# Kernel optimization log

Measured on AMD Instinct MI355X. Metric: run time of the kernel, lower is better.

The kernel has to match this reference:

```python
import jax, jax.numpy as jnp
import numpy as np

NUM_INPUTS, NUM_HIDDEN, NUM_OUTPUTS = 512, 1024, 35
T, B = 100, 512
N_HID_LAYERS = 4  # number of hidden Leaky layers (num_layers)
SLOPE = 25.0      # snntorch surrogate.fast_sigmoid default slope
BETA, THR = 0.95, 1.0


@jax.custom_vjp
def spike(x):
    # Heaviside forward, fast-sigmoid surrogate backward
    return (x > 0).astype(x.dtype)

def _spike_fwd(x):
    return (x > 0).astype(x.dtype), x

def _spike_bwd(x, g):
    return (g / (SLOPE * jnp.abs(x) + 1.0) ** 2,)

spike.defvjp(_spike_fwd, _spike_bwd)


def leaky(x, mem, beta, thr):
    # snntorch Leaky, reset_mechanism='subtract':
    # reset computed from PREVIOUS mem (detached), then decay+input, then fire
    reset = jax.lax.stop_gradient((mem - thr > 0).astype(x.dtype))
    mem = jnp.clip(beta, 0.0, 1.0) * mem + x - reset * thr
    spk = spike(mem - thr)
    return spk, mem


def setup_inputs() -> dict:
    key = jax.random.key(0)
    ks = jax.random.split(key, 8)
    data = jax.random.normal(ks[0], (T, B, NUM_INPUTS), dtype=jnp.float32)
    s_in = 1.0 / np.sqrt(NUM_INPUTS)
    s_h = 1.0 / np.sqrt(NUM_HIDDEN)
    W_in = jax.random.uniform(ks[1], (NUM_HIDDEN, NUM_INPUTS), minval=-s_in, maxval=s_in, dtype=jnp.float32)
    b_in = jax.random.uniform(ks[2], (NUM_HIDDEN,), minval=-s_in, maxval=s_in, dtype=jnp.float32)
    W_h = jax.random.uniform(ks[3], (N_HID_LAYERS - 1, NUM_HIDDEN, NUM_HIDDEN), minval=-s_h, maxval=s_h, dtype=jnp.float32)
    b_h = jax.random.uniform(ks[4], (N_HID_LAYERS - 1, NUM_HIDDEN), minval=-s_h, maxval=s_h, dtype=jnp.float32)
    W_out = jax.random.uniform(ks[5], (NUM_OUTPUTS, NUM_HIDDEN), minval=-s_h, maxval=s_h, dtype=jnp.float32)
    b_out = jax.random.uniform(ks[6], (NUM_OUTPUTS,), minval=-s_h, maxval=s_h, dtype=jnp.float32)
    # learn_beta/learn_threshold: each Leaky holds its own (identically initialized) params
    beta_h = jnp.full((N_HID_LAYERS, NUM_HIDDEN), BETA, dtype=jnp.float32)
    thr_h = jnp.full((N_HID_LAYERS, NUM_HIDDEN), THR, dtype=jnp.float32)
    beta_o = jnp.full((NUM_OUTPUTS,), BETA, dtype=jnp.float32)
    thr_o = jnp.full((NUM_OUTPUTS,), THR, dtype=jnp.float32)
    return {"data": data, "W_in": W_in, "b_in": b_in, "W_h": W_h, "b_h": b_h,
            "W_out": W_out, "b_out": b_out, "beta_h": beta_h, "thr_h": thr_h,
            "beta_o": beta_o, "thr_o": thr_o, "timestep": 100}


def reference(data, W_in, b_in, W_h, b_h, W_out, b_out, beta_h, thr_h, beta_o, thr_o, timestep):
    n_hid = beta_h.shape[0]
    Bsz = data.shape[1]

    def step(mems, x_t):
        new_mems = []
        x = x_t @ W_in.T + b_in
        x, m = leaky(x, mems[0], beta_h[0], thr_h[0])
        new_mems.append(m)
        for i in range(n_hid - 1):
            z = x @ W_h[i].T + b_h[i]
            x, m = leaky(z, mems[i + 1], beta_h[i + 1], thr_h[i + 1])
            new_mems.append(m)
        z = x @ W_out.T + b_out
        spk, m = leaky(z, mems[n_hid], beta_o, thr_o)
        new_mems.append(m)
        return tuple(new_mems), spk

    mems0 = tuple([jnp.zeros((Bsz, NUM_HIDDEN), dtype=data.dtype) for _ in range(n_hid)]
                  + [jnp.zeros((Bsz, NUM_OUTPUTS), dtype=data.dtype)])
    _, spk_rec = jax.lax.scan(step, mems0, data[:timestep])
    return spk_rec  # [T, B, num_outputs]
```

## Files before the change

kernel.cpp:

```cpp
#include <hip/hip_runtime.h>
#include <hip/hip_bf16.h>


#define NB 512
#define NH 1024
#define NI 512
#define NO 35
#define TT 100
#define NT 8
#define BITFRAME 16384

typedef __bf16 bf16x8 __attribute__((ext_vector_type(8)));
typedef float f32x4 __attribute__((ext_vector_type(4)));
typedef int   i32x4 __attribute__((ext_vector_type(4)));

__device__ __forceinline__ size_t tiled_off(int row, int k, int KT) {
    return ((size_t)((row >> 4) * KT + (k >> 5)) * 64
            + (row & 15) + (((k >> 3) & 3) << 4)) * 8 + (k & 7);
}

__device__ __forceinline__ void leaky_upd(float zin, float mprev, float be, float th,
                                          float& mnew, float& spk) {
    float rs = (mprev - th > 0.0f) ? th : 0.0f;
    float bc = fminf(fmaxf(be, 0.0f), 1.0f);
    mnew = bc * mprev + zin - rs;
    spk  = (mnew - th > 0.0f) ? 1.0f : 0.0f;
}

#define WS_MEM123   0u
#define WS_MEM0     6291456u
#define WS_MEMO     8388608u
#define WS_FLAGS    8486912u
#define WS_GEN      8487936u
#define WS_RING0    8488192u
#define WS_RING1    9536768u
#define WS_RING2    10585344u
#define WS_RING3    11633920u
#define WS_W8       12682496u
#define WS_WIT      25265408u
#define WS_WOT      28411136u
#define WS_Z0       28706048u
#define STEP_BYTES  2097152u

__global__ __launch_bounds__(256)
void split_weights_i8(const float* __restrict__ W_h, signed char* __restrict__ W8) {
    const int id = blockIdx.x * 256 + threadIdx.x;
    const int layer = id >> 16;
    const int rem = id & 65535;
    const int n = rem >> 6;
    const int k0 = (rem & 63) << 4;
    const float* src = W_h + ((size_t)layer * NH + n) * NH + k0;
    const int kq = k0 >> 4;
    const int ck = kq >> 2;
    const int lane = (n & 15) | ((kq & 3) << 4);
    signed char* dstL = W8 + (size_t)layer * 4 * NH * NH;
    const size_t gb = ((size_t)(n >> 4) * 16 + ck) * 1024 + lane * 16;

    signed char q1[16], q2[16], q3[16], q4[16];
    #pragma unroll
    for (int j = 0; j < 16; ++j) {
        float w = src[j];
        float f1 = rintf(w * 0x1p11f);   float r1 = w  - f1 * 0x1p-11f;
        float f2 = rintf(r1 * 0x1p18f);  float r2 = r1 - f2 * 0x1p-18f;
        float f3 = rintf(r2 * 0x1p25f);  float r3 = r2 - f3 * 0x1p-25f;
        float f4 = rintf(r3 * 0x1p32f);
        q1[j] = (signed char)(int)f1; q2[j] = (signed char)(int)f2;
        q3[j] = (signed char)(int)f3; q4[j] = (signed char)(int)f4;
    }
    #pragma unroll
    for (int j = 0; j < 16; ++j) {
        dstL[(size_t)0 * 64 * 16384 + gb + j] = q1[j];
        dstL[(size_t)1 * 64 * 16384 + gb + j] = q2[j];
        dstL[(size_t)2 * 64 * 16384 + gb + j] = q3[j];
        dstL[(size_t)3 * 64 * 16384 + gb + j] = q4[j];
    }
}

__global__ __launch_bounds__(256)
void split_win(const float* __restrict__ W_in, __bf16* __restrict__ Wi_t) {
    const int id = blockIdx.x * 256 + threadIdx.x;
    const int n = id >> 6;
    const int k0 = (id & 63) << 3;
    const float* src = W_in + (size_t)n * NI + k0;
    const size_t PS = (size_t)NH * NI;
    const size_t off = tiled_off(n, k0, 16);
    bf16x8 p1, p2, p3;
    #pragma unroll
    for (int j = 0; j < 8; ++j) {
        float w = src[j];
        __bf16 a = (__bf16)w;  float r1 = w - (float)a;
        __bf16 b = (__bf16)r1; float r2 = r1 - (float)b;
        __bf16 c = (__bf16)r2;
        p1[j] = a; p2[j] = b; p3[j] = c;
    }
    *reinterpret_cast<bf16x8*>(Wi_t + 0 * PS + off) = p1;
    *reinterpret_cast<bf16x8*>(Wi_t + 1 * PS + off) = p2;
    *reinterpret_cast<bf16x8*>(Wi_t + 2 * PS + off) = p3;
}

__global__ __launch_bounds__(256)
void split_wout(const float* __restrict__ W_out, __bf16* __restrict__ Wo_t) {
    const int id = blockIdx.x * 256 + threadIdx.x;
    if (id >= 48 * 128) return;
    const int o = id >> 7;
    const int k0 = (id & 127) << 3;
    const size_t PS = (size_t)48 * NH;
    const size_t off = tiled_off(o, k0, 32);
    bf16x8 p1 = {}, p2 = {}, p3 = {};
    if (o < NO) {
        const float* src = W_out + (size_t)o * NH + k0;
        #pragma unroll
        for (int j = 0; j < 8; ++j) {
            float w = src[j];
            __bf16 a = (__bf16)w;  float r1 = w - (float)a;
            __bf16 b = (__bf16)r1; float r2 = r1 - (float)b;
            __bf16 c = (__bf16)r2;
            p1[j] = a; p2[j] = b; p3[j] = c;
        }
    }
    *reinterpret_cast<bf16x8*>(Wo_t + 0 * PS + off) = p1;
    *reinterpret_cast<bf16x8*>(Wo_t + 1 * PS + off) = p2;
    *reinterpret_cast<bf16x8*>(Wo_t + 2 * PS + off) = p3;
}

__global__ __launch_bounds__(256)
void z0_gemm(const float* __restrict__ X,
             const __bf16* __restrict__ Wi_t,
             const float* __restrict__ bias,
             float* __restrict__ Z0)
{
    const int tid = threadIdx.x;
    const int lane = tid & 63;
    const int w = tid >> 6;
    const int wm = w >> 1, wn = w & 1;
    const int m_base = blockIdx.y * 64 + wm * 32;
    const int n_base = blockIdx.x * 64 + wn * 32;
    const size_t PS = (size_t)NH * NI;

    f32x4 acc[2][2] = {};
    const float* asrc[2];
    #pragma unroll
    for (int mt = 0; mt < 2; ++mt)
        asrc[mt] = X + (size_t)(m_base + mt * 16 + (lane & 15)) * NI + ((lane >> 4) << 3);

    float4 c0[2], c1[2];
    #pragma unroll
    for (int mt = 0; mt < 2; ++mt) {
        c0[mt] = *reinterpret_cast<const float4*>(asrc[mt]);
        c1[mt] = *reinterpret_cast<const float4*>(asrc[mt] + 4);
    }

    for (int kt = 0; kt < 16; ++kt) {
        float4 n0[2], n1[2];
        if (kt < 15) {
            #pragma unroll
            for (int mt = 0; mt < 2; ++mt) {
                n0[mt] = *reinterpret_cast<const float4*>(asrc[mt] + (kt + 1) * 32);
                n1[mt] = *reinterpret_cast<const float4*>(asrc[mt] + (kt + 1) * 32 + 4);
            }
        }
        bf16x8 a1[2], a2[2], a3[2];
        #pragma unroll
        for (int mt = 0; mt < 2; ++mt) {
            float xv[8] = {c0[mt].x, c0[mt].y, c0[mt].z, c0[mt].w,
                           c1[mt].x, c1[mt].y, c1[mt].z, c1[mt].w};
            #pragma unroll
            for (int j = 0; j < 8; ++j) {
                float x = xv[j];
                __bf16 h1 = (__bf16)x;  float r1 = x - (float)h1;
                __bf16 h2 = (__bf16)r1; float r2 = r1 - (float)h2;
                __bf16 h3 = (__bf16)r2;
                a1[mt][j] = h1; a2[mt][j] = h2; a3[mt][j] = h3;
            }
        }
        #pragma unroll
        for (int nt = 0; nt < 2; ++nt) {
            const size_t bo = ((size_t)(((n_base >> 4) + nt) * 16 + kt) * 64 + lane) * 8;
            bf16x8 b1 = *reinterpret_cast<const bf16x8*>(Wi_t + bo);
            bf16x8 b2 = *reinterpret_cast<const bf16x8*>(Wi_t + PS + bo);
            bf16x8 b3 = *reinterpret_cast<const bf16x8*>(Wi_t + 2 * PS + bo);
            #pragma unroll
            for (int mt = 0; mt < 2; ++mt) {
                f32x4 A = acc[mt][nt];
                A = __builtin_amdgcn_mfma_f32_16x16x32_bf16(a1[mt], b1, A, 0, 0, 0);
                A = __builtin_amdgcn_mfma_f32_16x16x32_bf16(a1[mt], b2, A, 0, 0, 0);
                A = __builtin_amdgcn_mfma_f32_16x16x32_bf16(a2[mt], b1, A, 0, 0, 0);
                A = __builtin_amdgcn_mfma_f32_16x16x32_bf16(a2[mt], b2, A, 0, 0, 0);
                A = __builtin_amdgcn_mfma_f32_16x16x32_bf16(a1[mt], b3, A, 0, 0, 0);
                A = __builtin_amdgcn_mfma_f32_16x16x32_bf16(a3[mt], b1, A, 0, 0, 0);
                acc[mt][nt] = A;
            }
        }
        if (kt < 15) {
            #pragma unroll
            for (int mt = 0; mt < 2; ++mt) { c0[mt] = n0[mt]; c1[mt] = n1[mt]; }
        }
    }

    const int c = lane & 15;
    const int r0 = (lane >> 4) * 4;
    #pragma unroll
    for (int nt = 0; nt < 2; ++nt) {
        const int n = n_base + nt * 16 + c;
        const float bi = bias[n];
        #pragma unroll
        for (int mt = 0; mt < 2; ++mt) {
            #pragma unroll
            for (int r = 0; r < 4; ++r) {
                const int m = m_base + mt * 16 + r0 + r;
                const int tl = m >> 9, b = m & 511;
                Z0[(size_t)tl * (NB * NH) + tiled_off(b, n, 32)] = acc[mt][nt][r] + bi;
            }
        }
    }
}

__device__ __forceinline__ void gridbar(int* flags, int* gen, int target) {
    __syncthreads();
    if (threadIdx.x == 0) {
        __builtin_amdgcn_fence(__ATOMIC_RELEASE, "agent");
        __hip_atomic_store(&flags[blockIdx.x], target, __ATOMIC_RELAXED, __HIP_MEMORY_SCOPE_AGENT);
    }
    if (blockIdx.x == 0) {
        if (threadIdx.x < 64) {
            const int l = threadIdx.x;
            for (;;) {
                int v0 = __hip_atomic_load(&flags[l],       __ATOMIC_RELAXED, __HIP_MEMORY_SCOPE_AGENT);
                int v1 = __hip_atomic_load(&flags[l + 64],  __ATOMIC_RELAXED, __HIP_MEMORY_SCOPE_AGENT);
                int v2 = __hip_atomic_load(&flags[l + 128], __ATOMIC_RELAXED, __HIP_MEMORY_SCOPE_AGENT);
                int v3 = __hip_atomic_load(&flags[l + 192], __ATOMIC_RELAXED, __HIP_MEMORY_SCOPE_AGENT);
                int mn = min(min(v0, v1), min(v2, v3));
                if (__all(mn >= target)) break;
                __builtin_amdgcn_s_sleep(1);
            }
        }
        __syncthreads();
        if (threadIdx.x == 0) {
            __builtin_amdgcn_fence(__ATOMIC_ACQ_REL, "agent");
            __hip_atomic_store(gen, target, __ATOMIC_RELAXED, __HIP_MEMORY_SCOPE_AGENT);
        }
    } else if (threadIdx.x == 0) {
        while (__hip_atomic_load(gen, __ATOMIC_RELAXED, __HIP_MEMORY_SCOPE_AGENT) < target)
            __builtin_amdgcn_s_sleep(2);
    }
    __syncthreads();
    __builtin_amdgcn_fence(__ATOMIC_ACQUIRE, "agent");
}

template<int NS>
__device__ __forceinline__ void hidden_run_i8(
    const unsigned int* const* Xp, unsigned short* const* Yp,
    const signed char* Wl, int cs, int rh, int w, int lane,
    float (&memr)[2][2][4], const float (&bi)[2], const float (&be)[2],
    const float (&th)[2])
{
    const int row  = lane & 15;
    const int lg   = lane >> 4;
    const int wsel = lg >> 1;
    const int hsel = (lg & 1) * 16;

    i32x4 acc[NS][2][2][4] = {};

    unsigned int bw[NS][2];
    #pragma unroll
    for (int q = 0; q < NS; ++q)
        #pragma unroll
        for (int i = 0; i < 2; ++i)
            bw[q][i] = Xp[q][((rh * 16 + w * 2 + i) * 32 + wsel) * 16 + row];

    for (int ck = 0; ck < 16; ++ck) {
        unsigned int nb[NS][2];
        if (ck < 15) {
            #pragma unroll
            for (int q = 0; q < NS; ++q)
                #pragma unroll
                for (int i = 0; i < 2; ++i)
                    nb[q][i] = Xp[q][((rh * 16 + w * 2 + i) * 32 + (ck + 1) * 2 + wsel) * 16 + row];
        }
        i32x4 bf[8];
        #pragma unroll
        for (int pn = 0; pn < 8; ++pn)
            bf[pn] = *reinterpret_cast<const i32x4*>(Wl + pn * 16384 + ck * 1024 + lane * 16);

        #pragma unroll
        for (int q = 0; q < NS; ++q) {
            #pragma unroll
            for (int i = 0; i < 2; ++i) {
                unsigned int half = (bw[q][i] >> hsel) & 0xFFFFu;
                union { unsigned int u[4]; i32x4 v; } a;
                a.u[0] = (((half      ) & 0xFu) * 0x204081u) & 0x01010101u;
                a.u[1] = (((half >>  4) & 0xFu) * 0x204081u) & 0x01010101u;
                a.u[2] = (((half >>  8) & 0xFu) * 0x204081u) & 0x01010101u;
                a.u[3] = (((half >> 12) & 0xFu) * 0x204081u) & 0x01010101u;
                #pragma unroll
                for (int nt = 0; nt < 2; ++nt)
                    #pragma unroll
                    for (int p = 0; p < 4; ++p)
                        acc[q][i][nt][p] = __builtin_amdgcn_mfma_i32_16x16x64_i8(
                            a.v, bf[p * 2 + nt], acc[q][i][nt][p], 0, 0, 0);
            }
        }
        if (ck < 15) {
            #pragma unroll
            for (int q = 0; q < NS; ++q) { bw[q][0] = nb[q][0]; bw[q][1] = nb[q][1]; }
        }
    }

    #pragma unroll
    for (int q = 0; q < NS; ++q) {
        #pragma unroll
        for (int i = 0; i < 2; ++i) {
            #pragma unroll
            for (int nt = 0; nt < 2; ++nt) {
                #pragma unroll
                for (int r = 0; r < 4; ++r) {
                    float z = (float)acc[q][i][nt][3][r] * 0x1p-32f
                            + (float)acc[q][i][nt][2][r] * 0x1p-25f;
                    z += (float)acc[q][i][nt][1][r] * 0x1p-18f;
                    z += (float)acc[q][i][nt][0][r] * 0x1p-11f;
                    float mn, sp;
                    leaky_upd(z + bi[nt], memr[i][nt][r], be[nt], th[nt], mn, sp);
                    memr[i][nt][r] = mn;
                    unsigned long long bal = __ballot(sp != 0.0f);
                    if ((lane & 15) == 0) {
                        const int rr = (lane >> 4) * 4 + r;
                        Yp[q][(((rh * 16 + w * 2 + i) * 32 + cs) * 16 + rr) * 2 + nt] =
                            (unsigned short)((bal >> ((lane >> 4) * 16)) & 0xFFFFu);
                    }
                }
            }
        }
    }
}

__global__ __launch_bounds__(512, 1)
void snn_pipe(const float* __restrict__ Z0,
              const signed char* __restrict__ W8,
              const __bf16* __restrict__ Wo_t,
              const float* __restrict__ b_h,
              const float* __restrict__ b_out,
              const float* __restrict__ beta_h,
              const float* __restrict__ thr_h,
              const float* __restrict__ beta_o,
              const float* __restrict__ thr_o,
              float* __restrict__ mem123,
              float* __restrict__ mem0_g,
              float* __restrict__ memo_g,
              unsigned int* __restrict__ ring0, unsigned int* __restrict__ ring1,
              unsigned int* __restrict__ ring2, unsigned int* __restrict__ ring3,
              float* __restrict__ out,
              int* __restrict__ flags, int* __restrict__ gen,
              int t0, int tc)
{
    __shared__ signed char Wl[8 * 16 * 1024];
    __shared__ unsigned long long lut[16];

    const int blk  = blockIdx.x;
    const int tid  = threadIdx.x;
    const int lane = tid & 63;
    const int w    = tid >> 6;

    if (tid < 16) {
        unsigned int lo = ((tid & 1) ? 0x3F80u : 0u) | ((tid & 2) ? 0x3F800000u : 0u);
        unsigned int hi = ((tid & 4) ? 0x3F80u : 0u) | ((tid & 8) ? 0x3F800000u : 0u);
        lut[tid] = ((unsigned long long)hi << 32) | lo;
    }

    const int G = (tc + NT - 1) / NT;

    if (blk < 192) {
        const int ell = blk >> 6;
        const int cs  = (blk & 63) >> 1;
        const int rh  = blk & 1;
        {
            const signed char* Wsrc = W8 + (size_t)ell * 4 * NH * NH;
            for (int idx = tid; idx < 8 * 1024; idx += 512) {
                const int pn = idx >> 10, off = idx & 1023;
                const int p = pn >> 1, nt = pn & 1;
                *reinterpret_cast<int4*>(Wl + pn * 16384 + off * 16) =
                    *reinterpret_cast<const int4*>(
                        Wsrc + (size_t)(p * 64 + cs * 2 + nt) * 16384 + off * 16);
            }
        }

        const int c = lane & 15;
        const int r0v = (lane >> 4) * 4;
        float* memg = mem123 + (size_t)ell * (NB * NH);
        float bi[2], be[2], th[2];
        #pragma unroll
        for (int nt = 0; nt < 2; ++nt) {
            const int n = cs * 32 + nt * 16 + c;
            bi[nt] = b_h[ell * NH + n];
            be[nt] = beta_h[(ell + 1) * NH + n];
            th[nt] = thr_h[(ell + 1) * NH + n];
        }
        float memr[2][2][4];
        #pragma unroll
        for (int i = 0; i < 2; ++i)
            #pragma unroll
            for (int nt = 0; nt < 2; ++nt)
                #pragma unroll
                for (int r = 0; r < 4; ++r)
                    memr[i][nt][r] = memg[(size_t)(rh * 256 + (w * 2 + i) * 16 + r0v + r) * NH
                                          + cs * 32 + nt * 16 + c];

        const unsigned int* rin = (ell == 0) ? ring0 : (ell == 1) ? ring1 : ring2;
        unsigned int* rout      = (ell == 0) ? ring1 : (ell == 1) ? ring2 : ring3;

        __syncthreads();

        for (int p = 0; p < G + 4; ++p) {
            const int g = p - 1 - ell;
            if (g >= 0 && g < G) {
                const int sbase = g * NT;
                const int send  = (sbase + NT < tc) ? sbase + NT : tc;
                const int slot0 = (g & 1) * NT;
                int s = sbase;
                while (s < send) {
                    const int base = slot0 + (s - sbase);
                    const unsigned int* Xp[2];
                    unsigned short* Yp[2];
                    if (send - s >= 2) {
                        #pragma unroll
                        for (int q = 0; q < 2; ++q) {
                            Xp[q] = rin + (size_t)(base + q) * BITFRAME;
                            Yp[q] = (unsigned short*)(rout + (size_t)(base + q) * BITFRAME);
                        }
                        hidden_run_i8<2>(Xp, Yp, Wl, cs, rh, w, lane, memr, bi, be, th);
                        s += 2;
                    } else {
                        Xp[0] = rin + (size_t)base * BITFRAME;
                        Yp[0] = (unsigned short*)(rout + (size_t)base * BITFRAME);
                        hidden_run_i8<1>(Xp, Yp, Wl, cs, rh, w, lane, memr, bi, be, th);
                        s += 1;
                    }
                }
            }
            gridbar(flags, gen, p + 1);
        }

        #pragma unroll
        for (int i = 0; i < 2; ++i)
            #pragma unroll
            for (int nt = 0; nt < 2; ++nt)
                #pragma unroll
                for (int r = 0; r < 4; ++r)
                    memg[(size_t)(rh * 256 + (w * 2 + i) * 16 + r0v + r) * NH
                         + cs * 32 + nt * 16 + c] = memr[i][nt][r];
    } else if (blk < 224) {
        const bool outw = (w < 3);
        const int omt = blk - 192;
        const int ont = w;
        const int c = lane & 15, r0v = (lane >> 4) * 4;
        const int row = lane & 15, sh2 = (lane >> 4) * 8;
        const int oo = ont * 16 + c;
        const size_t OPS = (size_t)48 * NH;
        float mo[4] = {0.f, 0.f, 0.f, 0.f};
        float obi = 0.f, obe = 0.f, oth = 1.f;
        if (outw && oo < NO) {
            obi = b_out[oo]; obe = beta_o[oo]; oth = thr_o[oo];
            #pragma unroll
            for (int r = 0; r < 4; ++r) mo[r] = memo_g[(omt * 16 + r0v + r) * NO + oo];
        }
        __syncthreads();

        for (int p = 0; p < G + 4; ++p) {
            if (outw) {
                const int go = p - 4;
                if (go >= 0 && go < G) {
                    const int sbase = go * NT;
                    const int send  = (sbase + NT < tc) ? sbase + NT : tc;
                    const int slot0 = (go & 1) * NT;
                    for (int s = sbase; s < send; ++s) {
                        const unsigned int* Xw =
                            ring3 + (size_t)(slot0 + s - sbase) * BITFRAME;
                        f32x4 acc = {};
                        for (int kt = 0; kt < 32; ++kt) {
                            unsigned int by = (Xw[(omt * 32 + kt) * 16 + row] >> sh2) & 0xffu;
                            union { unsigned long long u[2]; bf16x8 v; } a;
                            a.u[0] = lut[by & 15u];
                            a.u[1] = lut[by >> 4];
                            const size_t bo = ((size_t)(ont * 32 + kt) * 64 + lane) * 8;
                            bf16x8 q1 = *reinterpret_cast<const bf16x8*>(Wo_t + bo);
                            bf16x8 q2 = *reinterpret_cast<const bf16x8*>(Wo_t + OPS + bo);
                            bf16x8 q3 = *reinterpret_cast<const bf16x8*>(Wo_t + 2 * OPS + bo);
                            acc = __builtin_amdgcn_mfma_f32_16x16x32_bf16(a.v, q1, acc, 0, 0, 0);
                            acc = __builtin_amdgcn_mfma_f32_16x16x32_bf16(a.v, q2, acc, 0, 0, 0);
                            acc = __builtin_amdgcn_mfma_f32_16x16x32_bf16(a.v, q3, acc, 0, 0, 0);
                        }
                        if (oo < NO) {
                            #pragma unroll
                            for (int r = 0; r < 4; ++r) {
                                float mn, sp;
                                leaky_upd(acc[r] + obi, mo[r], obe, oth, mn, sp);
                                mo[r] = mn;
                                out[((size_t)(t0 + s) * NB + omt * 16 + r0v + r) * NO + oo] = sp;
                            }
                        }
                    }
                }
            }
            gridbar(flags, gen, p + 1);
        }

        if (outw && oo < NO) {
            #pragma unroll
            for (int r = 0; r < 4; ++r) memo_g[(omt * 16 + r0v + r) * NO + oo] = mo[r];
        }
    } else {
        const int wi   = (blk - 224) * 512 + tid;
        const int mtb  = wi >> 9;
        const int ktb  = (wi >> 4) & 31;
        const int i0   = (mtb * 32 + ktb) * 512 + (wi & 15) * 8;

        float m0[32], be0[32], th0[32];
        #pragma unroll
        for (int byt = 0; byt < 4; ++byt)
            #pragma unroll
            for (int j = 0; j < 8; ++j) {
                m0[byt * 8 + j]  = mem0_g[i0 + byt * 128 + j];
                be0[byt * 8 + j] = beta_h[ktb * 32 + byt * 8 + j];
                th0[byt * 8 + j] = thr_h[ktb * 32 + byt * 8 + j];
            }
        __syncthreads();

        for (int p = 0; p < G + 4; ++p) {
            if (p < G) {
                const int sbase = p * NT;
                const int send  = (sbase + NT < tc) ? sbase + NT : tc;
                const int slot0 = (p & 1) * NT;
                for (int s = sbase; s < send; ++s) {
                    const float* zs = Z0 + (size_t)s * (NB * NH) + i0;
                    float4 zv[8];
                    #pragma unroll
                    for (int byt = 0; byt < 4; ++byt) {
                        zv[byt * 2]     = *reinterpret_cast<const float4*>(zs + byt * 128);
                        zv[byt * 2 + 1] = *reinterpret_cast<const float4*>(zs + byt * 128 + 4);
                    }
                    unsigned int bits = 0;
                    #pragma unroll
                    for (int e = 0; e < 32; ++e) {
                        float z = reinterpret_cast<const float*>(zv)[e];
                        float mn, sp;
                        leaky_upd(z, m0[e], be0[e], th0[e], mn, sp);
                        m0[e] = mn;
                        bits |= (sp != 0.0f ? 1u : 0u) << e;
                    }
                    ring0[(size_t)(slot0 + s - sbase) * BITFRAME + wi] = bits;
                }
            }
            gridbar(flags, gen, p + 1);
        }

        #pragma unroll
        for (int byt = 0; byt < 4; ++byt)
            #pragma unroll
            for (int j = 0; j < 8; ++j)
                mem0_g[i0 + byt * 128 + j] = m0[byt * 8 + j];
    }
}

extern "C" void kernel_launch(void* const* d_in, const int* in_sizes, int n_in,
                              void* d_out, int out_size, void* d_ws, size_t ws_size,
                              hipStream_t stream) {
    const float* data   = (const float*)d_in[0];
    const float* W_in   = (const float*)d_in[1];
    const float* b_in   = (const float*)d_in[2];
    const float* W_h    = (const float*)d_in[3];
    const float* b_h    = (const float*)d_in[4];
    const float* W_out  = (const float*)d_in[5];
    const float* b_out  = (const float*)d_in[6];
    const float* beta_h = (const float*)d_in[7];
    const float* thr_h  = (const float*)d_in[8];
    const float* beta_o = (const float*)d_in[9];
    const float* thr_o  = (const float*)d_in[10];
    float* out = (float*)d_out;

    char* ws = (char*)d_ws;
    float*        mem123 = (float*)(ws + WS_MEM123);
    float*        mem0_g = (float*)(ws + WS_MEM0);
    float*        memo_g = (float*)(ws + WS_MEMO);
    int*          flags  = (int*)(ws + WS_FLAGS);
    int*          gen    = (int*)(ws + WS_GEN);
    unsigned int* ring0  = (unsigned int*)(ws + WS_RING0);
    unsigned int* ring1  = (unsigned int*)(ws + WS_RING1);
    unsigned int* ring2  = (unsigned int*)(ws + WS_RING2);
    unsigned int* ring3  = (unsigned int*)(ws + WS_RING3);
    signed char*  W8     = (signed char*)(ws + WS_W8);
    __bf16*       Wi_t   = (__bf16*)(ws + WS_WIT);
    __bf16*       Wo_t   = (__bf16*)(ws + WS_WOT);
    float*        Z0     = (float*)(ws + WS_Z0);

    size_t avail = (ws_size > WS_Z0) ? (ws_size - WS_Z0) / STEP_BYTES : 1;
    int Tc = (int)(avail < 1 ? 1 : (avail > TT ? TT : avail));

    hipMemsetAsync(ws, 0, WS_FLAGS, stream);
    split_weights_i8<<<dim3(768), dim3(256), 0, stream>>>(W_h, W8);
    split_win<<<dim3(256), dim3(256), 0, stream>>>(W_in, Wi_t);
    split_wout<<<dim3(24), dim3(256), 0, stream>>>(W_out, Wo_t);

    for (int t0c = 0; t0c < TT; t0c += Tc) {
        const int tcc = (TT - t0c < Tc) ? (TT - t0c) : Tc;
        z0_gemm<<<dim3(NH / 64, tcc * (NB / 64)), dim3(256), 0, stream>>>(
            data + (size_t)t0c * NB * NI, Wi_t, b_in, Z0);
        hipMemsetAsync(ws + WS_FLAGS, 0, 1280, stream);
        snn_pipe<<<dim3(256), dim3(512), 0, stream>>>(
            Z0, W8, Wo_t, b_h, b_out, beta_h, thr_h, beta_o, thr_o,
            mem123, mem0_g, memo_g, ring0, ring1, ring2, ring3, out,
            flags, gen, t0c, tcc);
    }
}
```

Baseline: 1.679 ms.

## Switch hidden-layer int8 MFMA to 32x32x32 tiles and pair output timesteps

The hidden-layer int8 GEMM moves from 16x16x64 MFMA tiles to 32x32x32 tiles. This changes the weight pre-split layout, the LDS weight staging, the accumulator and membrane register layout, and the spike bit-packing, which now writes 32-bit words instead of 16-bit halves. Each wave now covers 32 rows by 32 columns per tile, which is meant to halve the B-operand LDS reads per MFMA and cut the activation unpacking done per matrix op. The output-layer loop also processes two timesteps per pass so each loaded W_out fragment is reused. The risk is higher accumulator register pressure (16-wide i32 accumulators for each of NS and 4 splits) and possible LDS bank conflicts in the new layout.

```diff
diff --git a/kernel.cpp b/kernel.cpp
--- a/kernel.cpp
+++ b/kernel.cpp
@@ -13,6 +13,7 @@
 typedef __bf16 bf16x8 __attribute__((ext_vector_type(8)));
 typedef float f32x4 __attribute__((ext_vector_type(4)));
 typedef int   i32x4 __attribute__((ext_vector_type(4)));
+typedef int   i32x16 __attribute__((ext_vector_type(16)));
 
 __device__ __forceinline__ size_t tiled_off(int row, int k, int KT) {
     return ((size_t)((row >> 4) * KT + (k >> 5)) * 64
@@ -48,13 +49,13 @@
     const int layer = id >> 16;
     const int rem = id & 65535;
     const int n = rem >> 6;
-    const int k0 = (rem & 63) << 4;
+    const int kq = rem & 63;
+    const int k0 = kq << 4;
     const float* src = W_h + ((size_t)layer * NH + n) * NH + k0;
-    const int kq = k0 >> 4;
-    const int ck = kq >> 2;
-    const int lane = (n & 15) | ((kq & 3) << 4);
+    const int ck = kq >> 1;
+    const int lane = (n & 31) | ((kq & 1) << 5);
+    const int g = n >> 5;
     signed char* dstL = W8 + (size_t)layer * 4 * NH * NH;
-    const size_t gb = ((size_t)(n >> 4) * 16 + ck) * 1024 + lane * 16;
 
     signed char q1[16], q2[16], q3[16], q4[16];
     #pragma unroll
@@ -69,10 +70,10 @@
     }
     #pragma unroll
     for (int j = 0; j < 16; ++j) {
-        dstL[(size_t)0 * 64 * 16384 + gb + j] = q1[j];
-        dstL[(size_t)1 * 64 * 16384 + gb + j] = q2[j];
-        dstL[(size_t)2 * 64 * 16384 + gb + j] = q3[j];
-        dstL[(size_t)3 * 64 * 16384 + gb + j] = q4[j];
+        dstL[((size_t)(0 * 32 + g) * 32 + ck) * 1024 + lane * 16 + j] = q1[j];
+        dstL[((size_t)(1 * 32 + g) * 32 + ck) * 1024 + lane * 16 + j] = q2[j];
+        dstL[((size_t)(2 * 32 + g) * 32 + ck) * 1024 + lane * 16 + j] = q3[j];
+        dstL[((size_t)(3 * 32 + g) * 32 + ck) * 1024 + lane * 16 + j] = q4[j];
     }
 }
 
@@ -249,85 +250,70 @@
 
 template<int NS>
 __device__ __forceinline__ void hidden_run_i8(
-    const unsigned int* const* Xp, unsigned short* const* Yp,
+    const unsigned int* const* Xp, unsigned int* const* Yp,
     const signed char* Wl, int cs, int rh, int w, int lane,
-    float (&memr)[2][2][4], const float (&bi)[2], const float (&be)[2],
-    const float (&th)[2])
+    float (&memr)[16], float bi, float be, float th)
 {
-    const int row  = lane & 15;
-    const int lg   = lane >> 4;
-    const int wsel = lg >> 1;
-    const int hsel = (lg & 1) * 16;
-
-    i32x4 acc[NS][2][2][4] = {};
-
-    unsigned int bw[NS][2];
+    const int r32  = lane & 31;
+    const int khal = lane >> 5;
+    const int gr   = rh * 256 + w * 32 + r32;
+    const int mt   = gr >> 4;
+    const int r16  = gr & 15;
+    const int hsh  = khal * 16;
+
+    i32x16 acc[NS][4] = {};
+    unsigned int bw[NS];
     #pragma unroll
     for (int q = 0; q < NS; ++q)
-        #pragma unroll
-        for (int i = 0; i < 2; ++i)
-            bw[q][i] = Xp[q][((rh * 16 + w * 2 + i) * 32 + wsel) * 16 + row];
-
-    for (int ck = 0; ck < 16; ++ck) {
-        unsigned int nb[NS][2];
-        if (ck < 15) {
+        bw[q] = Xp[q][(mt * 32) * 16 + r16];
+
+    for (int ck = 0; ck < 32; ++ck) {
+        unsigned int nb[NS];
+        if (ck < 31) {
             #pragma unroll
             for (int q = 0; q < NS; ++q)
-                #pragma unroll
-                for (int i = 0; i < 2; ++i)
-                    nb[q][i] = Xp[q][((rh * 16 + w * 2 + i) * 32 + (ck + 1) * 2 + wsel) * 16 + row];
-        }
-        i32x4 bf[8];
-        #pragma unroll
-        for (int pn = 0; pn < 8; ++pn)
-            bf[pn] = *reinterpret_cast<const i32x4*>(Wl + pn * 16384 + ck * 1024 + lane * 16);
+                nb[q] = Xp[q][(mt * 32 + ck + 1) * 16 + r16];
+        }
+        i32x4 bf[4];
+        #pragma unroll
+        for (int p = 0; p < 4; ++p)
+            bf[p] = *reinterpret_cast<const i32x4*>(Wl + (size_t)(p * 32 + ck) * 1024 + lane * 16);
 
         #pragma unroll
         for (int q = 0; q < NS; ++q) {
-            #pragma unroll
-            for (int i = 0; i < 2; ++i) {
-                unsigned int half = (bw[q][i] >> hsel) & 0xFFFFu;
-                union { unsigned int u[4]; i32x4 v; } a;
-                a.u[0] = (((half      ) & 0xFu) * 0x204081u) & 0x01010101u;
-                a.u[1] = (((half >>  4) & 0xFu) * 0x204081u) & 0x01010101u;
-                a.u[2] = (((half >>  8) & 0xFu) * 0x204081u) & 0x01010101u;
-                a.u[3] = (((half >> 12) & 0xFu) * 0x204081u) & 0x01010101u;
-                #pragma unroll
-                for (int nt = 0; nt < 2; ++nt)
-                    #pragma unroll
-                    for (int p = 0; p < 4; ++p)
-                        acc[q][i][nt][p] = __builtin_amdgcn_mfma_i32_16x16x64_i8(
-                            a.v, bf[p * 2 + nt], acc[q][i][nt][p], 0, 0, 0);
-            }
-        }
-        if (ck < 15) {
-            #pragma unroll
-            for (int q = 0; q < NS; ++q) { bw[q][0] = nb[q][0]; bw[q][1] = nb[q][1]; }
+            unsigned int half = (bw[q] >> hsh) & 0xFFFFu;
+            union { unsigned int u[4]; i32x4 v; } a;
+            a.u[0] = (((half      ) & 0xFu) * 0x204081u) & 0x01010101u;
+            a.u[1] = (((half >>  4) & 0xFu) * 0x204081u) & 0x01010101u;
+            a.u[2] = (((half >>  8) & 0xFu) * 0x204081u) & 0x01010101u;
+            a.u[3] = (((half >> 12) & 0xFu) * 0x204081u) & 0x01010101u;
+            #pragma unroll
+            for (int p = 0; p < 4; ++p)
+                acc[q][p] = __builtin_amdgcn_mfma_i32_32x32x32_i8(
+                    a.v, bf[p], acc[q][p], 0, 0, 0);
+        }
+        if (ck < 31) {
+            #pragma unroll
+            for (int q = 0; q < NS; ++q) bw[q] = nb[q];
         }
     }
 
     #pragma unroll
     for (int q = 0; q < NS; ++q) {
         #pragma unroll
-        for (int i = 0; i < 2; ++i) {
-            #pragma unroll
-            for (int nt = 0; nt < 2; ++nt) {
-                #pragma unroll
-                for (int r = 0; r < 4; ++r) {
-                    float z = (float)acc[q][i][nt][3][r] * 0x1p-32f
-                            + (float)acc[q][i][nt][2][r] * 0x1p-25f;
-                    z += (float)acc[q][i][nt][1][r] * 0x1p-18f;
-                    z += (float)acc[q][i][nt][0][r] * 0x1p-11f;
-                    float mn, sp;
-                    leaky_upd(z + bi[nt], memr[i][nt][r], be[nt], th[nt], mn, sp);
-                    memr[i][nt][r] = mn;
-                    unsigned long long bal = __ballot(sp != 0.0f);
-                    if ((lane & 15) == 0) {
-                        const int rr = (lane >> 4) * 4 + r;
-                        Yp[q][(((rh * 16 + w * 2 + i) * 32 + cs) * 16 + rr) * 2 + nt] =
-                            (unsigned short)((bal >> ((lane >> 4) * 16)) & 0xFFFFu);
-                    }
-                }
+        for (int r = 0; r < 16; ++r) {
+            float z = (float)acc[q][3][r] * 0x1p-32f
+                    + (float)acc[q][2][r] * 0x1p-25f;
+            z += (float)acc[q][1][r] * 0x1p-18f;
+            z += (float)acc[q][0][r] * 0x1p-11f;
+            float mn, sp;
+            leaky_upd(z + bi, memr[r], be, th, mn, sp);
+            memr[r] = mn;
+            unsigned long long bal = __ballot(sp != 0.0f);
+            if ((lane & 31) == 0) {
+                const int grow = rh * 256 + w * 32 + (r & 3) + 8 * (r >> 2) + 4 * khal;
+                Yp[q][((grow >> 4) * 32 + cs) * 16 + (grow & 15)] =
+                    (unsigned int)(bal >> (khal * 32));
             }
         }
     }
@@ -352,7 +338,7 @@
               int* __restrict__ flags, int* __restrict__ gen,
               int t0, int tc)
 {
-    __shared__ signed char Wl[8 * 16 * 1024];
+    __shared__ signed char Wl[4 * 32 * 1024];
     __shared__ unsigned long long lut[16];
 
     const int blk  = blockIdx.x;
@@ -373,36 +359,29 @@
         const int cs  = (blk & 63) >> 1;
         const int rh  = blk & 1;
         {
-            const signed char* Wsrc = W8 + (size_t)ell * 4 * NH * NH;
-            for (int idx = tid; idx < 8 * 1024; idx += 512) {
-                const int pn = idx >> 10, off = idx & 1023;
-                const int p = pn >> 1, nt = pn & 1;
-                *reinterpret_cast<int4*>(Wl + pn * 16384 + off * 16) =
+            const signed char* Wsrc = W8 + (size_t)ell * 4 * NH * NH
+                                         + (size_t)cs * 32768;
+            for (int idx = tid; idx < 8192; idx += 512) {
+                const int p = idx >> 11, off = idx & 2047;
+                *reinterpret_cast<int4*>(Wl + (size_t)p * 32768 + off * 16) =
                     *reinterpret_cast<const int4*>(
-                        Wsrc + (size_t)(p * 64 + cs * 2 + nt) * 16384 + off * 16);
-            }
-        }
-
-        const int c = lane & 15;
-        const int r0v = (lane >> 4) * 4;
+                        Wsrc + (size_t)p * 32 * 32768 + off * 16);
+            }
+        }
+
+        const int n = cs * 32 + (lane & 31);
+        const int khal = lane >> 5;
         float* memg = mem123 + (size_t)ell * (NB * NH);
-        float bi[2], be[2], th[2];
-        #pragma unroll
-        for (int nt = 0; nt < 2; ++nt) {
-            const int n = cs * 32 + nt * 16 + c;
-            bi[nt] = b_h[ell * NH + n];
-            be[nt] = beta_h[(ell + 1) * NH + n];
-            th[nt] = thr_h[(ell + 1) * NH + n];
-        }
-        float memr[2][2][4];
-        #pragma unroll
-        for (int i = 0; i < 2; ++i)
-            #pragma unroll
-            for (int nt = 0; nt < 2; ++nt)
-                #pragma unroll
-                for (int r = 0; r < 4; ++r)
-                    memr[i][nt][r] = memg[(size_t)(rh * 256 + (w * 2 + i) * 16 + r0v + r) * NH
-                                          + cs * 32 + nt * 16 + c];
+        const float bi = b_h[ell * NH + n];
+        const float be = beta_h[(ell + 1) * NH + n];
+        const float th = thr_h[(ell + 1) * NH + n];
+
+        float memr[16];
+        #pragma unroll
+        for (int r = 0; r < 16; ++r) {
+            const int grow = rh * 256 + w * 32 + (r & 3) + 8 * (r >> 2) + 4 * khal;
+            memr[r] = memg[(size_t)grow * NH + n];
+        }
 
         const unsigned int* rin = (ell == 0) ? ring0 : (ell == 1) ? ring1 : ring2;
         unsigned int* rout      = (ell == 0) ? ring1 : (ell == 1) ? ring2 : ring3;
@@ -419,18 +398,18 @@
                 while (s < send) {
                     const int base = slot0 + (s - sbase);
                     const unsigned int* Xp[2];
-                    unsigned short* Yp[2];
+                    unsigned int* Yp[2];
                     if (send - s >= 2) {
                         #pragma unroll
                         for (int q = 0; q < 2; ++q) {
                             Xp[q] = rin + (size_t)(base + q) * BITFRAME;
-                            Yp[q] = (unsigned short*)(rout + (size_t)(base + q) * BITFRAME);
+                            Yp[q] = rout + (size_t)(base + q) * BITFRAME;
                         }
                         hidden_run_i8<2>(Xp, Yp, Wl, cs, rh, w, lane, memr, bi, be, th);
                         s += 2;
                     } else {
                         Xp[0] = rin + (size_t)base * BITFRAME;
-                        Yp[0] = (unsigned short*)(rout + (size_t)base * BITFRAME);
+                        Yp[0] = rout + (size_t)base * BITFRAME;
                         hidden_run_i8<1>(Xp, Yp, Wl, cs, rh, w, lane, memr, bi, be, th);
                         s += 1;
                     }
@@ -440,13 +419,10 @@
         }
 
         #pragma unroll
-        for (int i = 0; i < 2; ++i)
-            #pragma unroll
-            for (int nt = 0; nt < 2; ++nt)
-                #pragma unroll
-                for (int r = 0; r < 4; ++r)
-                    memg[(size_t)(rh * 256 + (w * 2 + i) * 16 + r0v + r) * NH
-                         + cs * 32 + nt * 16 + c] = memr[i][nt][r];
+        for (int r = 0; r < 16; ++r) {
+            const int grow = rh * 256 + w * 32 + (r & 3) + 8 * (r >> 2) + 4 * khal;
+            memg[(size_t)grow * NH + n] = memr[r];
+        }
     } else if (blk < 224) {
         const bool outw = (w < 3);
         const int omt = blk - 192;
@@ -471,30 +447,53 @@
                     const int sbase = go * NT;
                     const int send  = (sbase + NT < tc) ? sbase + NT : tc;
                     const int slot0 = (go & 1) * NT;
-                    for (int s = sbase; s < send; ++s) {
-                        const unsigned int* Xw =
+                    for (int s = sbase; s < send; s += 2) {
+                        const bool pair = (s + 1 < send);
+                        const unsigned int* Xw0 =
                             ring3 + (size_t)(slot0 + s - sbase) * BITFRAME;
-                        f32x4 acc = {};
+                        const unsigned int* Xw1 = pair ?
+                            ring3 + (size_t)(slot0 + s + 1 - sbase) * BITFRAME : Xw0;
+                        f32x4 acc0 = {}, acc1 = {};
                         for (int kt = 0; kt < 32; ++kt) {
-                            unsigned int by = (Xw[(omt * 32 + kt) * 16 + row] >> sh2) & 0xffu;
-                            union { unsigned long long u[2]; bf16x8 v; } a;
-                            a.u[0] = lut[by & 15u];
-                            a.u[1] = lut[by >> 4];
                             const size_t bo = ((size_t)(ont * 32 + kt) * 64 + lane) * 8;
                             bf16x8 q1 = *reinterpret_cast<const bf16x8*>(Wo_t + bo);
                             bf16x8 q2 = *reinterpret_cast<const bf16x8*>(Wo_t + OPS + bo);
                             bf16x8 q3 = *reinterpret_cast<const bf16x8*>(Wo_t + 2 * OPS + bo);
-                            acc = __builtin_amdgcn_mfma_f32_16x16x32_bf16(a.v, q1, acc, 0, 0, 0);
-                            acc = __builtin_amdgcn_mfma_f32_16x16x32_bf16(a.v, q2, acc, 0, 0, 0);
-                            acc = __builtin_amdgcn_mfma_f32_16x16x32_bf16(a.v, q3, acc, 0, 0, 0);
+                            {
+                                unsigned int by = (Xw0[(omt * 32 + kt) * 16 + row] >> sh2) & 0xffu;
+                                union { unsigned long long u[2]; bf16x8 v; } a;
+                                a.u[0] = lut[by & 15u];
+                                a.u[1] = lut[by >> 4];
+                                acc0 = __builtin_amdgcn_mfma_f32_16x16x32_bf16(a.v, q1, acc0, 0, 0, 0);
+                                acc0 = __builtin_amdgcn_mfma_f32_16x16x32_bf16(a.v, q2, acc0, 0, 0, 0);
+                                acc0 = __builtin_amdgcn_mfma_f32_16x16x32_bf16(a.v, q3, acc0, 0, 0, 0);
+                            }
+                            if (pair) {
+                                unsigned int by = (Xw1[(omt * 32 + kt) * 16 + row] >> sh2) & 0xffu;
+                                union { unsigned long long u[2]; bf16x8 v; } a;
+                                a.u[0] = lut[by & 15u];
+                                a.u[1] = lut[by >> 4];
+                                acc1 = __builtin_amdgcn_mfma_f32_16x16x32_bf16(a.v, q1, acc1, 0, 0, 0);
+                                acc1 = __builtin_amdgcn_mfma_f32_16x16x32_bf16(a.v, q2, acc1, 0, 0, 0);
+                                acc1 = __builtin_amdgcn_mfma_f32_16x16x32_bf16(a.v, q3, acc1, 0, 0, 0);
+                            }
                         }
                         if (oo < NO) {
                             #pragma unroll
                             for (int r = 0; r < 4; ++r) {
                                 float mn, sp;
-                                leaky_upd(acc[r] + obi, mo[r], obe, oth, mn, sp);
+                                leaky_upd(acc0[r] + obi, mo[r], obe, oth, mn, sp);
                                 mo[r] = mn;
                                 out[((size_t)(t0 + s) * NB + omt * 16 + r0v + r) * NO + oo] = sp;
+                            }
+                            if (pair) {
+                                #pragma unroll
+                                for (int r = 0; r < 4; ++r) {
+                                    float mn, sp;
+                                    leaky_upd(acc1[r] + obi, mo[r], obe, oth, mn, sp);
+                                    mo[r] = mn;
+                                    out[((size_t)(t0 + s + 1) * NB + omt * 16 + r0v + r) * NO + oo] = sp;
+                                }
                             }
                         }
                     }
```

Result: slower. 1.841 ms (+9.7%).
